# Performance work log

Measured on AMD Instinct MI355X. Metric: run time of the kernel, lower is better.

Reference implementation:

```python
import jax, jax.numpy as jnp
import numpy as np

B, T, C, H = 4, 2048, 1024, 16
HD = C // H  # head dim = 64


def setup_inputs() -> dict:
    key = jax.random.key(0)
    ks = jax.random.split(key, 5)
    s = 1.0 / np.sqrt(C)
    return {
        "x": jax.random.normal(ks[0], (B, T, C), jnp.float32),
        "Wk": jax.random.normal(ks[1], (C, C), jnp.float32) * s,
        "bk": jnp.zeros((C,), jnp.float32),
        "Wq": jax.random.normal(ks[2], (C, C), jnp.float32) * s,
        "bq": jnp.zeros((C,), jnp.float32),
        "Wv": jax.random.normal(ks[3], (C, C), jnp.float32) * s,
        "bv": jnp.zeros((C,), jnp.float32),
        "Wp": jax.random.normal(ks[4], (C, C), jnp.float32) * s,
        "bp": jnp.zeros((C,), jnp.float32),
    }


def reference(x, Wk, bk, Wq, bq, Wv, bv, Wp, bp):
    # Linear(in, out): y = x @ W.T + b  (W stored as [out, in], torch convention)
    k = (x @ Wk.T + bk).reshape(B, T, H, HD).transpose(0, 2, 1, 3)  # [B,H,T,HD]
    q = (x @ Wq.T + bq).reshape(B, T, H, HD).transpose(0, 2, 1, 3)
    v = (x @ Wv.T + bv).reshape(B, T, H, HD).transpose(0, 2, 1, 3)
    scale = 1.0 / np.sqrt(HD)
    att = jnp.einsum("bhqd,bhkd->bhqk", q, k) * scale  # [B,H,T,T]
    causal = jnp.tril(jnp.ones((T, T), bool))
    att = jnp.where(causal[None, None, :, :], att, -jnp.inf)
    att = jax.nn.softmax(att, axis=-1)
    y = jnp.einsum("bhqk,bhkd->bhqd", att, v)  # [B,H,T,HD]
    y = y.transpose(0, 2, 1, 3).reshape(B, T, C)
    return y @ Wp.T + bp
```

## Files before the change

### kernel.cpp

```cpp
#include <hip/hip_runtime.h>
#include <hip/hip_bf16.h>
#include <cmath>

#define Tt 2048
#define Cc 1024
#define Hh 16
#define HDd 64

typedef __attribute__((ext_vector_type(8))) short short8;
typedef __attribute__((ext_vector_type(4))) float f32x4;

#define ASYNC16(gp, lp)                                       \
    __builtin_amdgcn_global_load_lds(                         \
        (const __attribute__((address_space(1))) void*)(gp),  \
        (__attribute__((address_space(3))) void*)(lp), 16, 0, 0)

__device__ __forceinline__ unsigned short f32_bf16(float f) {
    unsigned u = __float_as_uint(f);
    u += 0x7FFF + ((u >> 16) & 1);
    return (unsigned short)(u >> 16);
}
__device__ __forceinline__ unsigned short f32_bf16_rn(float f) {
    return (unsigned short)((__float_as_uint(f) + 0x8000u) >> 16);
}
__device__ __forceinline__ float fast_exp2(float x) {
#if __has_builtin(__builtin_amdgcn_exp2f)
    return __builtin_amdgcn_exp2f(x);
#else
    return exp2f(x);
#endif
}

__global__ __launch_bounds__(256) void cvt_all(
    const float* __restrict__ x, const float* __restrict__ a,
    const float* __restrict__ b, const float* __restrict__ c,
    const float* __restrict__ d, unsigned short* __restrict__ ox,
    unsigned short* __restrict__ oa, unsigned short* __restrict__ ob,
    unsigned short* __restrict__ oc, unsigned short* __restrict__ od) {
    const int id = blockIdx.x * 256 + threadIdx.x;
    const float* src; unsigned short* dst; int sub;
    if (id < 2097152) {
        src = x; dst = ox; sub = id;
    } else {
        const int wi = id - 2097152;
        const int which = wi >> 18;
        sub = wi & 262143;
        if (which == 0)      { src = a; dst = oa; }
        else if (which == 1) { src = b; dst = ob; }
        else if (which == 2) { src = c; dst = oc; }
        else                 { src = d; dst = od; }
    }
    float4 v = ((const float4*)src)[sub];
    ushort4 o;
    o.x = f32_bf16(v.x); o.y = f32_bf16(v.y);
    o.z = f32_bf16(v.z); o.w = f32_bf16(v.w);
    ((ushort4*)dst)[sub] = o;
}

__global__ __launch_bounds__(512, 2) void gemm_qkv8(
    const unsigned short* __restrict__ A,
    const unsigned short* __restrict__ Wcat,
    const float* __restrict__ bq, const float* __restrict__ bk,
    const float* __restrict__ bv,
    unsigned short* __restrict__ qout, unsigned short* __restrict__ kout,
    unsigned short* __restrict__ vout) {
    extern __shared__ unsigned short lds[];

    const int tid  = threadIdx.x;
    const int wid  = tid >> 6;
    const int lane = tid & 63;
    const int quad = lane >> 4;
    const int lr   = lane & 15;
    const int wr   = wid >> 2;
    const int wc   = wid & 3;

    const int id   = blockIdx.y * 8 + blockIdx.x;
    const int xcd  = id & 7;
    const int rank = id >> 3;
    const int by   = xcd * 4 + (rank >> 3);
    const int bx   = rank & 7;
    const int bm0  = by * 256;
    const int bn0  = bx * 256;

    const int srow  = wid * 8 + (lane >> 3);
    const int scol  = ((lane & 7) ^ (lane >> 3)) * 8;
    const int sldso = wid * 512;

    const int a_r   = wr * 64 + lr;
    const int b_r   = wc * 32 + lr;
    const int slot0 = (quad ^ (lr & 7)) * 8;
    const int slot1 = ((quad ^ 4) ^ (lr & 7)) * 8;

    f32x4 acc[8][4];
    const f32x4 zero = {0.f, 0.f, 0.f, 0.f};
#pragma unroll
    for (int i = 0; i < 8; ++i)
#pragma unroll
        for (int j = 0; j < 4; ++j) acc[i][j] = zero;

    short8 areg[4][2];
    short8 breg[2][2][2];

#define STG(S, BUF, REG, GB, GROW)                                          \
    do {                                                                    \
        if ((S) < 16) {                                                     \
            unsigned short* lb = lds + ((BUF) * 4 + (REG)) * 8192 + sldso;  \
            const unsigned short* gp =                                      \
                (GB) + (size_t)((GROW) + srow) * Cc + (S) * 64 + scol;      \
            ASYNC16(gp, lb);                                                \
            ASYNC16(gp + (size_t)64 * Cc, lb + 4096);                       \
        }                                                                   \
    } while (0)

#define LDA(mh)                                                             \
    do {                                                                    \
        const unsigned short* ab = bufb + (mh) * 8192;                      \
        _Pragma("unroll") for (int mf = 0; mf < 4; ++mf) {                  \
            areg[mf][0] = *(const short8*)(ab + (a_r + mf * 16) * 64 + slot0); \
            areg[mf][1] = *(const short8*)(ab + (a_r + mf * 16) * 64 + slot1); \
        }                                                                   \
    } while (0)

#define LDB(nh)                                                             \
    do {                                                                    \
        const unsigned short* bb = bufb + (2 + (nh)) * 8192;                \
        _Pragma("unroll") for (int nf = 0; nf < 2; ++nf) {                  \
            breg[nh][nf][0] = *(const short8*)(bb + (b_r + nf * 16) * 64 + slot0); \
            breg[nh][nf][1] = *(const short8*)(bb + (b_r + nf * 16) * 64 + slot1); \
        }                                                                   \
    } while (0)

#define MFMA_PHASE(mh, nh)                                                  \
    _Pragma("unroll") for (int mf = 0; mf < 4; ++mf)                        \
    _Pragma("unroll") for (int nf = 0; nf < 2; ++nf) {                      \
        acc[(mh)*4+mf][(nh)*2+nf] = __builtin_amdgcn_mfma_f32_16x16x32_bf16( \
            areg[mf][0], breg[nh][nf][0], acc[(mh)*4+mf][(nh)*2+nf], 0,0,0); \
        acc[(mh)*4+mf][(nh)*2+nf] = __builtin_amdgcn_mfma_f32_16x16x32_bf16( \
            areg[mf][1], breg[nh][nf][1], acc[(mh)*4+mf][(nh)*2+nf], 0,0,0); \
    }

#define TILE(T, BC, WN)                                                     \
    {                                                                       \
        const unsigned short* bufb = lds + (BC) * 32768;                    \
        LDA(0);                                                             \
        LDB(0);                                                             \
        STG((T) + 1, (BC) ^ 1, 1, A, bm0 + 128);                            \
        __builtin_amdgcn_s_barrier();                                       \
        asm volatile("s_waitcnt lgkmcnt(0)" ::: "memory");                  \
        __builtin_amdgcn_s_setprio(1);                                      \
        MFMA_PHASE(0, 0);                                                   \
        __builtin_amdgcn_s_setprio(0);                                      \
        __builtin_amdgcn_s_barrier();                                       \
        LDB(1);                                                             \
        STG((T) + 1, (BC) ^ 1, 3, Wcat, bn0 + 128);                         \
        __builtin_amdgcn_s_barrier();                                       \
        asm volatile("s_waitcnt lgkmcnt(0)" ::: "memory");                  \
        __builtin_amdgcn_s_setprio(1);                                      \
        MFMA_PHASE(0, 1);                                                   \
        __builtin_amdgcn_s_setprio(0);                                      \
        __builtin_amdgcn_s_barrier();                                       \
        LDA(1);                                                             \
        STG((T) + 2, (BC), 0, A, bm0);                                      \
        __builtin_amdgcn_s_barrier();                                       \
        asm volatile("s_waitcnt lgkmcnt(0)" ::: "memory");                  \
        __builtin_amdgcn_s_setprio(1);                                      \
        MFMA_PHASE(1, 0);                                                   \
        __builtin_amdgcn_s_setprio(0);                                      \
        __builtin_amdgcn_s_barrier();                                       \
        STG((T) + 2, (BC), 2, Wcat, bn0);                                   \
        __builtin_amdgcn_s_barrier();                                       \
        __builtin_amdgcn_s_setprio(1);                                      \
        MFMA_PHASE(1, 1);                                                   \
        __builtin_amdgcn_s_setprio(0);                                      \
        asm volatile("s_waitcnt vmcnt(" #WN ")" ::: "memory");              \
        __builtin_amdgcn_s_barrier();                                       \
    }

    STG(0, 0, 0, A, bm0);
    STG(0, 0, 1, A, bm0 + 128);
    STG(0, 0, 2, Wcat, bn0);
    STG(0, 0, 3, Wcat, bn0 + 128);
    STG(1, 1, 0, A, bm0);
    STG(1, 1, 2, Wcat, bn0);
    asm volatile("s_waitcnt vmcnt(4)" ::: "memory");
    __builtin_amdgcn_s_barrier();

    for (int t2 = 0; t2 < 7; ++t2) {
        const int T0 = t2 * 2;
        TILE(T0, 0, 4);
        TILE(T0 + 1, 1, 4);
    }
    TILE(14, 0, 0);
    TILE(15, 1, 0);

#undef TILE
#undef MFMA_PHASE
#undef LDB
#undef LDA
#undef STG

    const int which = bn0 >> 10;
    const float* bias = (which == 0) ? bq : bk;
    unsigned short* outp = (which == 0) ? qout : kout;
    const float scale = (which == 0) ? 0.1803368801111204f : 1.0f;
    const int nb = bn0 & 1023;
    (void)bv; (void)vout;

#pragma unroll
    for (int nh = 0; nh < 2; ++nh)
#pragma unroll
        for (int nf = 0; nf < 2; ++nf) {
            const int nl = nb + nh * 128 + wc * 32 + nf * 16 + lr;
            const float bvv = bias[nl];
            const int h = nl >> 6, hd = nl & 63;
#pragma unroll
            for (int mh = 0; mh < 2; ++mh)
#pragma unroll
                for (int mf = 0; mf < 4; ++mf) {
                    const f32x4 a = acc[mh * 4 + mf][nh * 2 + nf];
                    const int m0 = bm0 + mh * 128 + wr * 64 + mf * 16 + quad * 4;
                    const int b = m0 >> 11, t0 = m0 & 2047;
#pragma unroll
                    for (int r = 0; r < 4; ++r) {
                        outp[(((size_t)(b * Hh + h)) * Tt + t0 + r) * HDd + hd] =
                            f32_bf16_rn((a[r] + bvv) * scale);
                    }
                }
        }
}

__global__ __launch_bounds__(512, 2) void gemm_v8(
    const unsigned short* __restrict__ A,
    const unsigned short* __restrict__ Wcat,
    const float* __restrict__ bv,
    unsigned short* __restrict__ vout) {
    extern __shared__ unsigned short lds[];

    const int tid  = threadIdx.x;
    const int wid  = tid >> 6;
    const int lane = tid & 63;
    const int quad = lane >> 4;
    const int lr   = lane & 15;
    const int wr   = wid >> 2;
    const int wc   = wid & 3;

    const int id   = blockIdx.y * 8 + blockIdx.x;
    const int xcd  = id & 7;
    const int rank = id >> 3;
    const int by   = xcd * 4 + (rank >> 3);
    const int bx   = rank & 7;
    const int bm0  = by * 256;
    const int wrow0 = 2048 + bx * 128;

    const int srow  = wid * 8 + (lane >> 3);
    const int scol  = ((lane & 7) ^ (lane >> 3)) * 8;
    const int sldso = wid * 512;

    const int a_r   = wr * 64 + lr;
    const int b_r2  = (wc & 1) * 32 + lr;
    const int breg_off = 16384 + (wc >> 1) * 4096;
    const int slot0 = (quad ^ (lr & 7)) * 8;
    const int slot1 = ((quad ^ 4) ^ (lr & 7)) * 8;

    f32x4 acc[8][2];
    const f32x4 zero = {0.f, 0.f, 0.f, 0.f};
#pragma unroll
    for (int i = 0; i < 8; ++i)
#pragma unroll
        for (int j = 0; j < 2; ++j) acc[i][j] = zero;

    short8 areg[4][2];
    short8 breg[2][2];

#define STGAV(S, BUF, REG_OFF, GROW)                                        \
    do {                                                                    \
        if ((S) < 16) {                                                     \
            unsigned short* lb = lds + (BUF) * 24576 + (REG_OFF) + sldso;   \
            const unsigned short* gp =                                      \
                A + (size_t)(bm0 + (GROW) + srow) * Cc + (S) * 64 + scol;   \
            ASYNC16(gp, lb);                                                \
            ASYNC16(gp + (size_t)64 * Cc, lb + 4096);                       \
        }                                                                   \
    } while (0)

#define STGBV(S, BUF, REG_OFF, NROW)                                        \
    do {                                                                    \
        if ((S) < 16) {                                                     \
            unsigned short* lb = lds + (BUF) * 24576 + (REG_OFF) + sldso;   \
            const unsigned short* gp =                                      \
                Wcat + (size_t)(wrow0 + (NROW) + srow) * Cc + (S) * 64 + scol; \
            ASYNC16(gp, lb);                                                \
        }                                                                   \
    } while (0)

#define LDA_V(mh)                                                           \
    do {                                                                    \
        const unsigned short* ab = bufb + (mh) * 8192;                      \
        _Pragma("unroll") for (int mf = 0; mf < 4; ++mf) {                  \
            areg[mf][0] = *(const short8*)(ab + (a_r + mf * 16) * 64 + slot0); \
            areg[mf][1] = *(const short8*)(ab + (a_r + mf * 16) * 64 + slot1); \
        }                                                                   \
    } while (0)

#define LDB_V                                                               \
    do {                                                                    \
        const unsigned short* bb = bufb + breg_off;                         \
        _Pragma("unroll") for (int nf = 0; nf < 2; ++nf) {                  \
            breg[nf][0] = *(const short8*)(bb + (b_r2 + nf * 16) * 64 + slot0); \
            breg[nf][1] = *(const short8*)(bb + (b_r2 + nf * 16) * 64 + slot1); \
        }                                                                   \
    } while (0)

#define MFMA_V(mh)                                                          \
    _Pragma("unroll") for (int mf = 0; mf < 4; ++mf)                        \
    _Pragma("unroll") for (int nf = 0; nf < 2; ++nf) {                      \
        acc[(mh)*4+mf][nf] = __builtin_amdgcn_mfma_f32_16x16x32_bf16(       \
            areg[mf][0], breg[nf][0], acc[(mh)*4+mf][nf], 0, 0, 0);         \
        acc[(mh)*4+mf][nf] = __builtin_amdgcn_mfma_f32_16x16x32_bf16(       \
            areg[mf][1], breg[nf][1], acc[(mh)*4+mf][nf], 0, 0, 0);         \
    }

#define TILE_V(T, BC, WN)                                                   \
    {                                                                       \
        const unsigned short* bufb = lds + (BC) * 24576;                    \
        LDA_V(0);                                                           \
        LDB_V;                                                              \
        STGAV((T) + 1, (BC) ^ 1, 8192, 128);                                \
        STGBV((T) + 1, (BC) ^ 1, 20480, 64);                                \
        __builtin_amdgcn_s_barrier();                                       \
        asm volatile("s_waitcnt lgkmcnt(0)" ::: "memory");                  \
        __builtin_amdgcn_s_setprio(1);                                      \
        MFMA_V(0);                                                          \
        __builtin_amdgcn_s_setprio(0);                                      \
        __builtin_amdgcn_s_barrier();                                       \
        LDA_V(1);                                                           \
        STGAV((T) + 2, (BC), 0, 0);                                         \
        STGBV((T) + 2, (BC), 16384, 0);                                     \
        __builtin_amdgcn_s_barrier();                                       \
        asm volatile("s_waitcnt lgkmcnt(0)" ::: "memory");                  \
        __builtin_amdgcn_s_setprio(1);                                      \
        MFMA_V(1);                                                          \
        __builtin_amdgcn_s_setprio(0);                                      \
        asm volatile("s_waitcnt vmcnt(" #WN ")" ::: "memory");              \
        __builtin_amdgcn_s_barrier();                                       \
    }

    STGAV(0, 0, 0, 0);
    STGAV(0, 0, 8192, 128);
    STGBV(0, 0, 16384, 0);
    STGBV(0, 0, 20480, 64);
    STGAV(1, 1, 0, 0);
    STGBV(1, 1, 16384, 0);
    asm volatile("s_waitcnt vmcnt(3)" ::: "memory");
    __builtin_amdgcn_s_barrier();

    for (int t2 = 0; t2 < 7; ++t2) {
        const int T0 = t2 * 2;
        TILE_V(T0, 0, 3);
        TILE_V(T0 + 1, 1, 3);
    }
    TILE_V(14, 0, 0);
    TILE_V(15, 1, 0);

#undef TILE_V
#undef MFMA_V
#undef LDB_V
#undef LDA_V
#undef STGBV
#undef STGAV

#pragma unroll
    for (int nf = 0; nf < 2; ++nf) {
        const int nl = (wrow0 - 2048) + wc * 32 + nf * 16 + lr;
        const float bvv = bv[nl];
        const int h = nl >> 6, hd = nl & 63;
#pragma unroll
        for (int mh = 0; mh < 2; ++mh)
#pragma unroll
            for (int mf = 0; mf < 4; ++mf) {
                const f32x4 a = acc[mh * 4 + mf][nf];
                const int m0 = bm0 + mh * 128 + wr * 64 + mf * 16 + quad * 4;
                const int b = m0 >> 11, t0 = m0 & 2047;
                ushort4 pk;
                pk.x = f32_bf16_rn(a[0] + bvv);
                pk.y = f32_bf16_rn(a[1] + bvv);
                pk.z = f32_bf16_rn(a[2] + bvv);
                pk.w = f32_bf16_rn(a[3] + bvv);
                *(ushort4*)(vout + (((size_t)(b * Hh + h)) * HDd + hd) * Tt + t0) = pk;
            }
    }
}

__global__ __launch_bounds__(512, 2) void gemm_proj8(
    const unsigned short* __restrict__ A,
    const unsigned short* __restrict__ W,
    const float* __restrict__ bias,
    float* __restrict__ out) {
    extern __shared__ unsigned short lds[];

    const int tid  = threadIdx.x;
    const int wid  = tid >> 6;
    const int lane = tid & 63;
    const int quad = lane >> 4;
    const int lr   = lane & 15;
    const int wr   = wid >> 2;
    const int wc   = wid & 3;

    const int id   = blockIdx.y * 8 + blockIdx.x;
    const int xcd  = id & 7;
    const int rank = id >> 3;
    const int by   = xcd * 4 + (rank >> 3);
    const int bx   = rank & 7;
    const int bm0  = by * 256;
    const int bn0  = bx * 128;

    const int srow  = wid * 8 + (lane >> 3);
    const int scol  = ((lane & 7) ^ (lane >> 3)) * 8;
    const int sldso = wid * 512;

    const int a_r   = wr * 64 + lr;
    const int b_r2  = (wc & 1) * 32 + lr;
    const int breg_off = 16384 + (wc >> 1) * 4096;
    const int slot0 = (quad ^ (lr & 7)) * 8;
    const int slot1 = ((quad ^ 4) ^ (lr & 7)) * 8;

    f32x4 acc[8][2];
    const f32x4 zero = {0.f, 0.f, 0.f, 0.f};
#pragma unroll
    for (int i = 0; i < 8; ++i)
#pragma unroll
        for (int j = 0; j < 2; ++j) acc[i][j] = zero;

    short8 areg[4][2];
    short8 breg[2][2];

#define STGA(S, BUF, REG_OFF, GROW)                                         \
    do {                                                                    \
        if ((S) < 16) {                                                     \
            unsigned short* lb = lds + (BUF) * 24576 + (REG_OFF) + sldso;   \
            const unsigned short* gp =                                      \
                A + (size_t)(bm0 + (GROW) + srow) * Cc + (S) * 64 + scol;   \
            ASYNC16(gp, lb);                                                \
            ASYNC16(gp + (size_t)64 * Cc, lb + 4096);                       \
        }                                                                   \
    } while (0)

#define STGB(S, BUF, REG_OFF, NROW)                                         \
    do {                                                                    \
        if ((S) < 16) {                                                     \
            unsigned short* lb = lds + (BUF) * 24576 + (REG_OFF) + sldso;   \
            const unsigned short* gp =                                      \
                W + (size_t)(bn0 + (NROW) + srow) * Cc + (S) * 64 + scol;   \
            ASYNC16(gp, lb);                                                \
        }                                                                   \
    } while (0)

#define LDA_P(mh)                                                           \
    do {                                                                    \
        const unsigned short* ab = bufb + (mh) * 8192;                      \
        _Pragma("unroll") for (int mf = 0; mf < 4; ++mf) {                  \
            areg[mf][0] = *(const short8*)(ab + (a_r + mf * 16) * 64 + slot0); \
            areg[mf][1] = *(const short8*)(ab + (a_r + mf * 16) * 64 + slot1); \
        }                                                                   \
    } while (0)

#define LDB_P                                                               \
    do {                                                                    \
        const unsigned short* bb = bufb + breg_off;                         \
        _Pragma("unroll") for (int nf = 0; nf < 2; ++nf) {                  \
            breg[nf][0] = *(const short8*)(bb + (b_r2 + nf * 16) * 64 + slot0); \
            breg[nf][1] = *(const short8*)(bb + (b_r2 + nf * 16) * 64 + slot1); \
        }                                                                   \
    } while (0)

#define MFMA_P(mh)                                                          \
    _Pragma("unroll") for (int mf = 0; mf < 4; ++mf)                        \
    _Pragma("unroll") for (int nf = 0; nf < 2; ++nf) {                      \
        acc[(mh)*4+mf][nf] = __builtin_amdgcn_mfma_f32_16x16x32_bf16(       \
            areg[mf][0], breg[nf][0], acc[(mh)*4+mf][nf], 0, 0, 0);         \
        acc[(mh)*4+mf][nf] = __builtin_amdgcn_mfma_f32_16x16x32_bf16(       \
            areg[mf][1], breg[nf][1], acc[(mh)*4+mf][nf], 0, 0, 0);         \
    }

#define TILE_P(T, BC, WN)                                                   \
    {                                                                       \
        const unsigned short* bufb = lds + (BC) * 24576;                    \
        LDA_P(0);                                                           \
        LDB_P;                                                              \
        STGA((T) + 1, (BC) ^ 1, 8192, 128);                                 \
        STGB((T) + 1, (BC) ^ 1, 20480, 64);                                 \
        __builtin_amdgcn_s_barrier();                                       \
        asm volatile("s_waitcnt lgkmcnt(0)" ::: "memory");                  \
        __builtin_amdgcn_s_setprio(1);                                      \
        MFMA_P(0);                                                          \
        __builtin_amdgcn_s_setprio(0);                                      \
        __builtin_amdgcn_s_barrier();                                       \
        LDA_P(1);                                                           \
        STGA((T) + 2, (BC), 0, 0);                                          \
        STGB((T) + 2, (BC), 16384, 0);                                      \
        __builtin_amdgcn_s_barrier();                                       \
        asm volatile("s_waitcnt lgkmcnt(0)" ::: "memory");                  \
        __builtin_amdgcn_s_setprio(1);                                      \
        MFMA_P(1);                                                          \
        __builtin_amdgcn_s_setprio(0);                                      \
        asm volatile("s_waitcnt vmcnt(" #WN ")" ::: "memory");              \
        __builtin_amdgcn_s_barrier();                                       \
    }

    STGA(0, 0, 0, 0);
    STGA(0, 0, 8192, 128);
    STGB(0, 0, 16384, 0);
    STGB(0, 0, 20480, 64);
    STGA(1, 1, 0, 0);
    STGB(1, 1, 16384, 0);
    asm volatile("s_waitcnt vmcnt(3)" ::: "memory");
    __builtin_amdgcn_s_barrier();

    for (int t2 = 0; t2 < 7; ++t2) {
        const int T0 = t2 * 2;
        TILE_P(T0, 0, 3);
        TILE_P(T0 + 1, 1, 3);
    }
    TILE_P(14, 0, 0);
    TILE_P(15, 1, 0);

#undef TILE_P
#undef MFMA_P
#undef LDB_P
#undef LDA_P
#undef STGB
#undef STGA

#pragma unroll
    for (int nf = 0; nf < 2; ++nf) {
        const int n = bn0 + wc * 32 + nf * 16 + lr;
        const float bvv = bias[n];
#pragma unroll
        for (int mh = 0; mh < 2; ++mh)
#pragma unroll
            for (int mf = 0; mf < 4; ++mf) {
                const f32x4 a = acc[mh * 4 + mf][nf];
                const int m0 = bm0 + mh * 128 + wr * 64 + mf * 16 + quad * 4;
#pragma unroll
                for (int r = 0; r < 4; ++r)
                    out[(size_t)(m0 + r) * Cc + n] = a[r] + bvv;
            }
    }
}

__global__ __launch_bounds__(256, 4) void attn(const unsigned short* __restrict__ q,
                                               const unsigned short* __restrict__ k,
                                               const unsigned short* __restrict__ vt,
                                               unsigned short* __restrict__ y) {
    __shared__ unsigned short sK[2][64 * 64];
    __shared__ unsigned short sV[2][64 * 64];
    __shared__ unsigned short sP[4][16 * 64];

    const int tid  = threadIdx.x;
    const int wid  = tid >> 6;
    const int lane = tid & 63;
    const int quad = lane >> 4;
    const int lr   = lane & 15;

    const int bh = blockIdx.x;
    const int qx = blockIdx.y;
    const size_t headq = (size_t)bh * Tt * HDd;
    const unsigned short* kg = k + headq;
    const unsigned short* vg = vt + headq;
    const int b = bh >> 4, h = bh & 15;

    const int g_r = lane >> 3;
    const int g_c = ((lane & 7) ^ g_r) * 8;
    const unsigned short* kst = kg + (size_t)(wid * 16 + g_r) * HDd + g_c;
    const unsigned short* vst = vg + (size_t)(wid * 16 + g_r) * Tt + g_c;
    unsigned short* dK0 = sK[0] + wid * 1024;
    unsigned short* dK1 = sK[1] + wid * 1024;
    unsigned short* dV0 = sV[0] + wid * 1024;
    unsigned short* dV1 = sV[1] + wid * 1024;

#define STAGE_KV(BUF, KB)                                                   \
    do {                                                                    \
        unsigned short* dK = (BUF) ? dK1 : dK0;                             \
        unsigned short* dV = (BUF) ? dV1 : dV0;                             \
        ASYNC16(kst + (size_t)(KB) * HDd,       dK);                        \
        ASYNC16(kst + (size_t)((KB) + 8) * HDd, dK + 512);                  \
        ASYNC16(vst + (KB),                     dV);                        \
        ASYNC16(vst + (size_t)8 * Tt + (KB),    dV + 512);                  \
    } while (0)

    const int fr_off = lr * 64 + ((quad ^ (lr & 7)) * 8);
    const int hq8 = (((lr >> 3) ^ ((quad & 1) << 2)) * 8);
    const int pwb = quad * 256 + (lr & 7);
    unsigned short* sPw = sP[wid];

    const f32x4 zero = {0.f, 0.f, 0.f, 0.f};

    for (int pass = 0; pass < 2; ++pass) {
        const int qt = pass ? (31 - qx) : qx;
        const int qb = qt * 64;
        const int ntiles = qt + 1;

        const unsigned short* qp = q + headq + (size_t)(qb + wid * 16 + lr) * HDd;
        const short8 qf0 = *(const short8*)(qp + quad * 8);
        const short8 qf1 = *(const short8*)(qp + 32 + quad * 8);

        f32x4 o[4];
        float l_run[4];
#pragma unroll
        for (int i = 0; i < 4; i++) { o[i] = zero; l_run[i] = 0.f; }

        STAGE_KV(0, 0);
        __syncthreads();

        for (int kt = 0; kt < ntiles; ++kt) {
            const int cur = kt & 1;
            if (kt + 1 < ntiles) STAGE_KV(cur ^ 1, (kt + 1) * 64);

            const unsigned short* bK = sK[cur];
            const unsigned short* bV = sV[cur];

            short8 kf[4][2];
#pragma unroll
            for (int nt = 0; nt < 4; nt++) {
                kf[nt][0] = *(const short8*)(bK + nt * 1024 + fr_off);
                kf[nt][1] = *(const short8*)(bK + nt * 1024 + (fr_off ^ 32));
            }

            f32x4 sc[4];
            __builtin_amdgcn_s_setprio(1);
#pragma unroll
            for (int nt = 0; nt < 4; nt++) {
                f32x4 a = __builtin_amdgcn_mfma_f32_16x16x32_bf16(qf0, kf[nt][0], zero, 0, 0, 0);
                sc[nt]  = __builtin_amdgcn_mfma_f32_16x16x32_bf16(qf1, kf[nt][1], a, 0, 0, 0);
            }
            __builtin_amdgcn_s_setprio(0);

            short8 vf[4][2];
#pragma unroll
            for (int nt = 0; nt < 4; nt++) {
                vf[nt][0] = *(const short8*)(bV + nt * 1024 + fr_off);
                vf[nt][1] = *(const short8*)(bV + nt * 1024 + (fr_off ^ 32));
            }

            if (kt == qt) {
#pragma unroll
                for (int nt = 0; nt < 4; nt++)
#pragma unroll
                    for (int r = 0; r < 4; r++)
                        sc[nt][r] = (nt * 16 + lr <= wid * 16 + quad * 4 + r)
                                        ? sc[nt][r] : -INFINITY;
            }

#pragma unroll
            for (int nt = 0; nt < 4; nt++)
#pragma unroll
                for (int r = 0; r < 4; r++) {
                    const float p = fast_exp2(sc[nt][r]);
                    l_run[r] += p;
                    sPw[pwb + r * 64 + ((nt * 16 ^ r * 8) ^ hq8)] = f32_bf16_rn(p);
                }

            const short8 pa0 = *(const short8*)(sPw + fr_off);
            const short8 pa1 = *(const short8*)(sPw + (fr_off ^ 32));

            __builtin_amdgcn_s_setprio(1);
#pragma unroll
            for (int nt = 0; nt < 4; nt++) {
                o[nt] = __builtin_amdgcn_mfma_f32_16x16x32_bf16(pa0, vf[nt][0], o[nt], 0, 0, 0);
                o[nt] = __builtin_amdgcn_mfma_f32_16x16x32_bf16(pa1, vf[nt][1], o[nt], 0, 0, 0);
            }
            __builtin_amdgcn_s_setprio(0);

            __syncthreads();
        }

#pragma unroll
        for (int r = 0; r < 4; r++) {
            float ls = l_run[r];
            ls += __shfl_xor(ls, 1);
            ls += __shfl_xor(ls, 2);
            ls += __shfl_xor(ls, 4);
            ls += __shfl_xor(ls, 8);
            const float inv = 1.0f / ls;
            const int t = qb + wid * 16 + quad * 4 + r;
#pragma unroll
            for (int nt = 0; nt < 4; nt++) {
                const int dim = nt * 16 + lr;
                y[((size_t)(b * Tt + t)) * Cc + h * HDd + dim] =
                    f32_bf16_rn(o[nt][r] * inv);
            }
        }
    }
#undef STAGE_KV
}

extern "C" void kernel_launch(void* const* d_in, const int* in_sizes, int n_in,
                              void* d_out, int out_size, void* d_ws, size_t ws_size,
                              hipStream_t stream) {
    const float* x  = (const float*)d_in[0];
    const float* Wk = (const float*)d_in[1];
    const float* bk = (const float*)d_in[2];
    const float* Wq = (const float*)d_in[3];
    const float* bq = (const float*)d_in[4];
    const float* Wv = (const float*)d_in[5];
    const float* bv = (const float*)d_in[6];
    const float* Wp = (const float*)d_in[7];
    const float* bp = (const float*)d_in[8];
    float* out = (float*)d_out;

    char* ws = (char*)d_ws;
    size_t off = 0;
    auto alloc = [&](size_t bytes) { char* p = ws + off; off += bytes; return p; };
    const size_t MK = (size_t)8192 * 1024;
    const size_t NK = (size_t)1024 * 1024;
    unsigned short* xb   = (unsigned short*)alloc(MK * 2);
    unsigned short* Wcat = (unsigned short*)alloc(3 * NK * 2);
    unsigned short* Wqb  = Wcat;
    unsigned short* Wkb  = Wcat + NK;
    unsigned short* Wvb  = Wcat + 2 * NK;
    unsigned short* Wpb  = (unsigned short*)alloc(NK * 2);
    unsigned short* qh   = (unsigned short*)alloc(MK * 2);
    unsigned short* kh   = (unsigned short*)alloc(MK * 2);
    unsigned short* vth  = (unsigned short*)alloc(MK * 2);
    unsigned short* ya   = (unsigned short*)alloc(MK * 2);

    static bool lds_attr_set = false;
    if (!lds_attr_set) {
        (void)hipFuncSetAttribute((const void*)gemm_qkv8,
                                  hipFuncAttributeMaxDynamicSharedMemorySize,
                                  131072);
        (void)hipFuncSetAttribute((const void*)gemm_v8,
                                  hipFuncAttributeMaxDynamicSharedMemorySize,
                                  98304);
        (void)hipFuncSetAttribute((const void*)gemm_proj8,
                                  hipFuncAttributeMaxDynamicSharedMemorySize,
                                  98304);
        lds_attr_set = true;
    }

    cvt_all<<<12288, 256, 0, stream>>>(x, Wq, Wk, Wv, Wp, xb, Wqb, Wkb, Wvb, Wpb);

    gemm_qkv8<<<dim3(8, 32), 512, 131072, stream>>>(xb, Wcat, bq, bk, bv, qh, kh, vth);
    gemm_v8<<<dim3(8, 32), 512, 98304, stream>>>(xb, Wcat, bv, vth);

    attn<<<dim3(64, 16), 256, 0, stream>>>(qh, kh, vth, ya);

    gemm_proj8<<<dim3(8, 32), 512, 98304, stream>>>(ya, Wpb, bp, out);
}
```

Baseline: 243.4 us.

## Rewrite attention inner loop with 32x32 MFMA and register-only P transpose

Switches the attention kernel from 16x16x32 to 32x32x16 bf16 MFMA, computing S^T = K·Q^T so the probabilities can be packed with v_cvt_pk_bf16_f32 and rearranged with v_permlane32_swap instead of a round trip through LDS. Each block now handles 128-query tiles, with 32 rows per wave, and the grid halves in y. Waves skip key tiles above their causal diagonal. The launch bound drops to 2 blocks per CU, which frees registers for the larger accumulators but lowers occupancy.

```diff
diff --git a/kernel.cpp b/kernel.cpp
--- a/kernel.cpp
+++ b/kernel.cpp
@@ -9,6 +9,7 @@
 
 typedef __attribute__((ext_vector_type(8))) short short8;
 typedef __attribute__((ext_vector_type(4))) float f32x4;
+typedef __attribute__((ext_vector_type(16))) float f32x16;
 
 #define ASYNC16(gp, lp)                                       \
     __builtin_amdgcn_global_load_lds(                         \
@@ -548,19 +549,19 @@
     }
 }
 
-__global__ __launch_bounds__(256, 4) void attn(const unsigned short* __restrict__ q,
+__global__ __launch_bounds__(256, 2) void attn(const unsigned short* __restrict__ q,
                                                const unsigned short* __restrict__ k,
                                                const unsigned short* __restrict__ vt,
                                                unsigned short* __restrict__ y) {
     __shared__ unsigned short sK[2][64 * 64];
     __shared__ unsigned short sV[2][64 * 64];
-    __shared__ unsigned short sP[4][16 * 64];
 
     const int tid  = threadIdx.x;
     const int wid  = tid >> 6;
     const int lane = tid & 63;
-    const int quad = lane >> 4;
-    const int lr   = lane & 15;
+    const int l31  = lane & 31;
+    const int hb   = lane >> 5;
+    const int x7   = lane & 7;
 
     const int bh = blockIdx.x;
     const int qx = blockIdx.y;
@@ -588,26 +589,31 @@
         ASYNC16(vst + (size_t)8 * Tt + (KB),    dV + 512);                  \
     } while (0)
 
-    const int fr_off = lr * 64 + ((quad ^ (lr & 7)) * 8);
-    const int hq8 = (((lr >> 3) ^ ((quad & 1) << 2)) * 8);
-    const int pwb = quad * 256 + (lr & 7);
-    unsigned short* sPw = sP[wid];
-
-    const f32x4 zero = {0.f, 0.f, 0.f, 0.f};
+#define CVTPK(d, a, bb) asm("v_cvt_pk_bf16_f32 %0, %1, %2" : "=v"(d) : "v"(a), "v"(bb))
+#define PLSWAP(xx, yy)  asm("v_permlane32_swap_b32 %0, %1" : "+v"(xx), "+v"(yy))
+
+    const int frow = l31 * 64;
+
+    const f32x16 zero16 = {0.f,0.f,0.f,0.f,0.f,0.f,0.f,0.f,
+                           0.f,0.f,0.f,0.f,0.f,0.f,0.f,0.f};
+
+    const int nwoff = 1 + (wid >> 1);
 
     for (int pass = 0; pass < 2; ++pass) {
-        const int qt = pass ? (31 - qx) : qx;
-        const int qb = qt * 64;
-        const int ntiles = qt + 1;
-
-        const unsigned short* qp = q + headq + (size_t)(qb + wid * 16 + lr) * HDd;
-        const short8 qf0 = *(const short8*)(qp + quad * 8);
-        const short8 qf1 = *(const short8*)(qp + 32 + quad * 8);
-
-        f32x4 o[4];
-        float l_run[4];
-#pragma unroll
-        for (int i = 0; i < 4; i++) { o[i] = zero; l_run[i] = 0.f; }
+        const int qt = pass ? (15 - qx) : qx;
+        const int qb = qt * 128;
+        const int ntiles = 2 * qt + 2;
+        const int nw = 2 * qt + nwoff;
+
+        const unsigned short* qp =
+            q + headq + (size_t)(qb + wid * 32 + l31) * HDd;
+        short8 qf[4];
+#pragma unroll
+        for (int c = 0; c < 4; c++)
+            qf[c] = *(const short8*)(qp + c * 16 + hb * 8);
+
+        f32x16 o0 = zero16, o1 = zero16;
+        float l_run = 0.f;
 
         STAGE_KV(0, 0);
         __syncthreads();
@@ -616,82 +622,88 @@
             const int cur = kt & 1;
             if (kt + 1 < ntiles) STAGE_KV(cur ^ 1, (kt + 1) * 64);
 
-            const unsigned short* bK = sK[cur];
-            const unsigned short* bV = sV[cur];
-
-            short8 kf[4][2];
-#pragma unroll
-            for (int nt = 0; nt < 4; nt++) {
-                kf[nt][0] = *(const short8*)(bK + nt * 1024 + fr_off);
-                kf[nt][1] = *(const short8*)(bK + nt * 1024 + (fr_off ^ 32));
+            if (kt < nw) {
+                const unsigned short* bK = sK[cur];
+                const unsigned short* bV = sV[cur];
+
+                f32x16 p0 = zero16, p1 = zero16;
+                __builtin_amdgcn_s_setprio(1);
+#pragma unroll
+                for (int c = 0; c < 4; c++) {
+                    const int cs = ((2 * c + hb) ^ x7) * 8;
+                    short8 kf0 = *(const short8*)(bK + frow + cs);
+                    short8 kf1 = *(const short8*)(bK + 2048 + frow + cs);
+                    p0 = __builtin_amdgcn_mfma_f32_32x32x16_bf16(kf0, qf[c], p0, 0, 0, 0);
+                    p1 = __builtin_amdgcn_mfma_f32_32x32x16_bf16(kf1, qf[c], p1, 0, 0, 0);
+                }
+                __builtin_amdgcn_s_setprio(0);
+
+                if (kt == nw - 1 || kt == ntiles - 1) {
+                    const int qd = qb + wid * 32 + l31 - kt * 64 - 4 * hb;
+#pragma unroll
+                    for (int r = 0; r < 16; r++) {
+                        const int kb0 = (r & 3) + 8 * (r >> 2);
+                        p0[r] = (kb0 <= qd) ? p0[r] : -INFINITY;
+                        p1[r] = (kb0 + 32 <= qd) ? p1[r] : -INFINITY;
+                    }
+                }
+
+                float lacc = 0.f;
+#pragma unroll
+                for (int r = 0; r < 16; r++) {
+                    p0[r] = fast_exp2(p0[r]); lacc += p0[r];
+                    p1[r] = fast_exp2(p1[r]); lacc += p1[r];
+                }
+                l_run += lacc;
+
+                unsigned w0[4][2], w1[4][2];
+#pragma unroll
+                for (int g = 0; g < 4; g++) {
+                    CVTPK(w0[g][0], p0[4 * g + 0], p0[4 * g + 1]);
+                    CVTPK(w0[g][1], p0[4 * g + 2], p0[4 * g + 3]);
+                    CVTPK(w1[g][0], p1[4 * g + 0], p1[4 * g + 1]);
+                    CVTPK(w1[g][1], p1[4 * g + 2], p1[4 * g + 3]);
+                }
+
+                __builtin_amdgcn_s_setprio(1);
+#pragma unroll
+                for (int kc = 0; kc < 4; kc++) {
+                    unsigned x0, x1, y0, y1;
+                    if (kc == 0)      { x0 = w0[0][0]; x1 = w0[0][1]; y0 = w0[1][0]; y1 = w0[1][1]; }
+                    else if (kc == 1) { x0 = w0[2][0]; x1 = w0[2][1]; y0 = w0[3][0]; y1 = w0[3][1]; }
+                    else if (kc == 2) { x0 = w1[0][0]; x1 = w1[0][1]; y0 = w1[1][0]; y1 = w1[1][1]; }
+                    else              { x0 = w1[2][0]; x1 = w1[2][1]; y0 = w1[3][0]; y1 = w1[3][1]; }
+                    PLSWAP(x0, y0);
+                    PLSWAP(x1, y1);
+                    union { unsigned u[4]; short8 s; } pu;
+                    pu.u[0] = x0; pu.u[1] = x1; pu.u[2] = y0; pu.u[3] = y1;
+
+                    const int vs = ((2 * kc + hb) ^ x7) * 8;
+                    short8 vf0 = *(const short8*)(bV + frow + vs);
+                    short8 vf1 = *(const short8*)(bV + 2048 + frow + vs);
+                    o0 = __builtin_amdgcn_mfma_f32_32x32x16_bf16(pu.s, vf0, o0, 0, 0, 0);
+                    o1 = __builtin_amdgcn_mfma_f32_32x32x16_bf16(pu.s, vf1, o1, 0, 0, 0);
+                }
+                __builtin_amdgcn_s_setprio(0);
             }
-
-            f32x4 sc[4];
-            __builtin_amdgcn_s_setprio(1);
-#pragma unroll
-            for (int nt = 0; nt < 4; nt++) {
-                f32x4 a = __builtin_amdgcn_mfma_f32_16x16x32_bf16(qf0, kf[nt][0], zero, 0, 0, 0);
-                sc[nt]  = __builtin_amdgcn_mfma_f32_16x16x32_bf16(qf1, kf[nt][1], a, 0, 0, 0);
-            }
-            __builtin_amdgcn_s_setprio(0);
-
-            short8 vf[4][2];
-#pragma unroll
-            for (int nt = 0; nt < 4; nt++) {
-                vf[nt][0] = *(const short8*)(bV + nt * 1024 + fr_off);
-                vf[nt][1] = *(const short8*)(bV + nt * 1024 + (fr_off ^ 32));
-            }
-
-            if (kt == qt) {
-#pragma unroll
-                for (int nt = 0; nt < 4; nt++)
-#pragma unroll
-                    for (int r = 0; r < 4; r++)
-                        sc[nt][r] = (nt * 16 + lr <= wid * 16 + quad * 4 + r)
-                                        ? sc[nt][r] : -INFINITY;
-            }
-
-#pragma unroll
-            for (int nt = 0; nt < 4; nt++)
-#pragma unroll
-                for (int r = 0; r < 4; r++) {
-                    const float p = fast_exp2(sc[nt][r]);
-                    l_run[r] += p;
-                    sPw[pwb + r * 64 + ((nt * 16 ^ r * 8) ^ hq8)] = f32_bf16_rn(p);
-                }
-
-            const short8 pa0 = *(const short8*)(sPw + fr_off);
-            const short8 pa1 = *(const short8*)(sPw + (fr_off ^ 32));
-
-            __builtin_amdgcn_s_setprio(1);
-#pragma unroll
-            for (int nt = 0; nt < 4; nt++) {
-                o[nt] = __builtin_amdgcn_mfma_f32_16x16x32_bf16(pa0, vf[nt][0], o[nt], 0, 0, 0);
-                o[nt] = __builtin_amdgcn_mfma_f32_16x16x32_bf16(pa1, vf[nt][1], o[nt], 0, 0, 0);
-            }
-            __builtin_amdgcn_s_setprio(0);
 
             __syncthreads();
         }
 
-#pragma unroll
-        for (int r = 0; r < 4; r++) {
-            float ls = l_run[r];
-            ls += __shfl_xor(ls, 1);
-            ls += __shfl_xor(ls, 2);
-            ls += __shfl_xor(ls, 4);
-            ls += __shfl_xor(ls, 8);
-            const float inv = 1.0f / ls;
-            const int t = qb + wid * 16 + quad * 4 + r;
-#pragma unroll
-            for (int nt = 0; nt < 4; nt++) {
-                const int dim = nt * 16 + lr;
-                y[((size_t)(b * Tt + t)) * Cc + h * HDd + dim] =
-                    f32_bf16_rn(o[nt][r] * inv);
-            }
+        l_run += __shfl_xor(l_run, 32);
+        const float inv = 1.0f / l_run;
+        unsigned short* yp = y + (size_t)(b * Tt + qb + wid * 32) * Cc + h * HDd;
+#pragma unroll
+        for (int r = 0; r < 16; r++) {
+            const int qr = (r & 3) + 8 * (r >> 2) + 4 * hb;
+            const float invr = __shfl(inv, qr);
+            yp[(size_t)qr * Cc + l31]      = f32_bf16_rn(o0[r] * invr);
+            yp[(size_t)qr * Cc + 32 + l31] = f32_bf16_rn(o1[r] * invr);
         }
     }
 #undef STAGE_KV
+#undef CVTPK
+#undef PLSWAP
 }
 
 extern "C" void kernel_launch(void* const* d_in, const int* in_sizes, int n_in,
@@ -743,7 +755,7 @@
     gemm_qkv8<<<dim3(8, 32), 512, 131072, stream>>>(xb, Wcat, bq, bk, bv, qh, kh, vth);
     gemm_v8<<<dim3(8, 32), 512, 98304, stream>>>(xb, Wcat, bv, vth);
 
-    attn<<<dim3(64, 16), 256, 0, stream>>>(qh, kh, vth, ya);
+    attn<<<dim3(64, 8), 256, 0, stream>>>(qh, kh, vth, ya);
 
     gemm_proj8<<<dim3(8, 32), 512, 98304, stream>>>(ya, Wpb, bp, out);
 }
```

After: 229.2 us. 1.06x faster.
